# Optimization experiments

Hardware: AMD Instinct MI355X
Metric: run time of the kernel (lower is better)

The kernel has to match this reference:

```python
import jax, jax.numpy as jnp
from jax import lax
import numpy as np

K = 3  # kernel size for both convs


def setup_inputs() -> dict:
    key = jax.random.key(0)
    k1, k2, k3, k4, k5 = jax.random.split(key, 5)
    x = jax.random.normal(k1, (8, 3, 384, 384), dtype=jnp.float32)
    # offset-producing conv: 18 = 2*3*3 offset channels for a 3x3 deform kernel
    w1 = jax.random.normal(k2, (18, 3, K, K), dtype=jnp.float32) * 0.05
    b1 = jax.random.normal(k3, (18,), dtype=jnp.float32) * 0.05
    # deformable conv weight/bias: in=3, out=3, 3x3
    w2 = jax.random.normal(k4, (3, 3, K, K), dtype=jnp.float32) * 0.2
    b2 = jax.random.normal(k5, (3,), dtype=jnp.float32) * 0.05
    return {"x": x, "w1": w1, "b1": b1, "w2": w2, "b2": b2}


def _deform_conv2d(x, offset, w, b):
    # x: [B,C,H,W], offset: [B, 2*K*K, Ho, Wo] (per-tap (dy,dx) interleaved),
    # w: [Co,C,K,K], b: [Co]. stride=1, pad=0, dilation=1, zero-padding bilinear.
    B, C, H, W = x.shape
    KK = K * K
    Ho, Wo = H - (K - 1), W - (K - 1)
    off = offset.reshape(B, KK, 2, Ho, Wo)
    dy, dx = off[:, :, 0], off[:, :, 1]                      # [B,KK,Ho,Wo]

    kh = jnp.repeat(jnp.arange(K, dtype=jnp.float32), K)     # [KK] kernel row
    kw = jnp.tile(jnp.arange(K, dtype=jnp.float32), K)       # [KK] kernel col
    base_y = jnp.arange(Ho, dtype=jnp.float32)[None, :, None] + kh[:, None, None]  # [KK,Ho,1]
    base_x = jnp.arange(Wo, dtype=jnp.float32)[None, None, :] + kw[:, None, None]  # [KK,1,Wo]
    py = base_y[None] + dy                                   # [B,KK,Ho,Wo]
    px = base_x[None] + dx

    y0 = jnp.floor(py)
    x0 = jnp.floor(px)
    wy = py - y0
    wx = px - x0

    x_flat = x.reshape(B, C, H * W)
    N = KK * Ho * Wo

    def gather_corner(yc, xc, wgt):
        valid = (yc >= 0) & (yc <= H - 1) & (xc >= 0) & (xc <= W - 1)
        yi = jnp.clip(yc, 0, H - 1).astype(jnp.int32)
        xi = jnp.clip(xc, 0, W - 1).astype(jnp.int32)
        idx = (yi * W + xi).reshape(B, 1, N)
        g = jnp.take_along_axis(x_flat, idx, axis=2)          # [B,C,N]
        return g * (wgt * valid.astype(x.dtype)).reshape(B, 1, N)

    val = gather_corner(y0, x0, (1 - wy) * (1 - wx))
    val = val + gather_corner(y0, x0 + 1, (1 - wy) * wx)
    val = val + gather_corner(y0 + 1, x0, wy * (1 - wx))
    val = val + gather_corner(y0 + 1, x0 + 1, wy * wx)
    val = val.reshape(B, C, KK, Ho, Wo)

    out = jnp.einsum('bckhw,ock->bohw', val, w.reshape(w.shape[0], C, KK))
    return out + b[None, :, None, None]


def reference(x, w1, b1, w2, b2):
    offset = lax.conv_general_dilated(
        x, w1, window_strides=(1, 1), padding='VALID',
        dimension_numbers=('NCHW', 'OIHW', 'NCHW')) + b1[None, :, None, None]
    return _deform_conv2d(x, offset, w2, b2)
```

## Files before the change

kernel.cpp:

```cpp
#include <hip/hip_runtime.h>


#define BB 8
#define HH 384
#define WW 384
#define HO 382
#define WO 382
#define HW (HH * WW)
#define TW 64
#define TH 4
#define TILES_X 6
#define TILES_Y 96
#define SROWS 11
#define SCOLS 72
#define SSTRIDE 73

typedef float v2f __attribute__((ext_vector_type(2), aligned(4)));
typedef float v4f __attribute__((ext_vector_type(4), aligned(16)));

static __device__ __forceinline__ v2f fma2(v2f a, v2f b, v2f c) {
    return __builtin_elementwise_fma(a, b, c);
}
static __device__ __forceinline__ v4f fma4(v4f a, v4f b, v4f c) {
    return __builtin_elementwise_fma(a, b, c);
}

__global__ __launch_bounds__(256) void deform_tiled(
    const float* __restrict__ x,
    const float* __restrict__ w1,
    const float* __restrict__ b1,
    const float* __restrict__ w2,
    const float* __restrict__ b2,
    float* __restrict__ out)
{
    __shared__ v4f  s_tile[SROWS * SSTRIDE];
    __shared__ float s_w1p[486];
    __shared__ float s_b1[18];
    __shared__ float s_w2p[54];
    __shared__ float s_w2s[27];
    __shared__ float s_b2[3];

    for (int i = threadIdx.x; i < 486; i += 256) {
        const int oc = i / 27, rem = i % 27, c = rem / 9, j = rem % 9;
        const int k = oc >> 1, comp = oc & 1;
        s_w1p[((j * 3 + c) * 9 + k) * 2 + comp] = w1[i];
    }
    if (threadIdx.x < 81) {
        const int i = threadIdx.x;
        const int o = i / 27, c = (i % 27) / 9, k = i % 9;
        if (o < 2) s_w2p[(k * 3 + c) * 2 + o] = w2[i];
        else       s_w2s[k * 3 + c] = w2[i];
    }
    if (threadIdx.x < 18) s_b1[threadIdx.x] = b1[threadIdx.x];
    if (threadIdx.x < 3)  s_b2[threadIdx.x] = b2[threadIdx.x];

    const int b  = blockIdx.x & 7;
    const int t  = blockIdx.x >> 3;
    const int tx = t % TILES_X;
    const int ty = t / TILES_X;
    const int w0 = tx * TW;
    const int r0 = ty * TH;

    const float* xp0 = x + (long)b * 3 * HW;
    const float* xp1 = xp0 + HW;
    const float* xp2 = xp0 + 2 * HW;

    const int gr0 = r0 - 2, gc0 = w0 - 2;
    for (int s = threadIdx.x; s < SROWS * SCOLS; s += 256) {
        const int sr = s / SCOLS, sc = s - sr * SCOLS;
        const int gy = min(max(gr0 + sr, 0), HH - 1);
        const int gx = min(max(gc0 + sc, 0), WW - 1);
        const int base = gy * WW + gx;
        v4f v;
        v.x = xp0[base];
        v.y = xp1[base];
        v.z = xp2[base];
        v.w = 0.f;
        s_tile[sr * SSTRIDE + sc] = v;
    }
    __syncthreads();

    const int wo_in = threadIdx.x & 63;
    const int ho_in = threadIdx.x >> 6;
    const int wo = w0 + wo_in;
    const int ho = r0 + ho_in;
    if (wo >= WO || ho >= HO) return;

    v2f off2[9];
#pragma unroll
    for (int k = 0; k < 9; ++k) {
        v2f v; v.x = s_b1[2 * k]; v.y = s_b1[2 * k + 1];
        off2[k] = v;
    }

    const v2f* w1p = (const v2f*)s_w1p;
#pragma unroll
    for (int j = 0; j < 9; ++j) {
        const int i = j / 3, jj = j % 3;
        const v4f q = s_tile[(ho_in + 2 + i) * SSTRIDE + (wo_in + 2 + jj)];
#pragma unroll
        for (int c = 0; c < 3; ++c) {
            const float xc = (c == 0) ? q.x : (c == 1) ? q.y : q.z;
            v2f xcv; xcv.x = xc; xcv.y = xc;
            const v2f* wrow = w1p + (j * 3 + c) * 9;
#pragma unroll
            for (int k = 0; k < 9; ++k)
                off2[k] = fma2(xcv, wrow[k], off2[k]);
        }
    }

    float acc0 = s_b2[0], acc1 = s_b2[1], acc2 = s_b2[2];
    const v2f* w2p = (const v2f*)s_w2p;

    const bool interior = (gr0 >= 0) & (gc0 >= 0) &
                          (gr0 + SROWS <= HH) & (gc0 + SCOLS <= WW);

    if (interior) {
#pragma unroll 1
        for (int k = 0; k < 9; ++k) {
            const int kh = k / 3, kw = k - kh * 3;
            v2f pos; pos.x = (float)(ho + kh); pos.y = (float)(wo + kw);
            pos += off2[k];
            const v2f fl = __builtin_elementwise_floor(pos);
            const v2f fr = pos - fl;
            const int y0 = (int)fl.x;
            const int x0 = (int)fl.y;

            const int ly0 = y0 - gr0;
            const int lx  = x0 - gc0;
            const bool inTile = ((unsigned)ly0 <= SROWS - 2) &
                                ((unsigned)lx  <= SCOLS - 2);

            float g00 = (1.f - fr.x) * (1.f - fr.y);
            float g01 = (1.f - fr.x) * fr.y;
            float g10 = fr.x * (1.f - fr.y);
            float g11 = fr.x * fr.y;

            const int cy0 = min(max(ly0, 0), SROWS - 2);
            const int cx  = min(max(lx, 0),  SCOLS - 2);
            const v4f* p0 = s_tile + cy0 * SSTRIDE + cx;
            const v4f* p1 = p0 + SSTRIDE;
            v4f q00 = p0[0], q01 = p0[1];
            v4f q10 = p1[0], q11 = p1[1];

            if (!inTile) {
                const int ry0 = min(max(y0, 0), HH - 1);
                const int ry1 = min(max(y0 + 1, 0), HH - 1);
                const int xbs = min(max(x0, 0), WW - 2);
                const bool vy0 = (y0 >= 0) & (y0 <= HH - 1);
                const bool vy1 = (y0 >= -1) & (y0 <= HH - 2);
                const bool vx0 = (x0 >= 0) & (x0 <= WW - 1);
                const bool vx1 = (x0 >= -1) & (x0 <= WW - 2);
                const float wy0m = vy0 ? (1.f - fr.x) : 0.f;
                const float wy1m = vy1 ? fr.x : 0.f;
                const float wx0m = vx0 ? (1.f - fr.y) : 0.f;
                const float wx1m = vx1 ? fr.y : 0.f;
                const bool selA = (x0 >= WW - 1);
                const bool selB = (x0 >= 0);
                const float e0 = (selA ? 0.f : wx0m) + (selB ? 0.f : wx1m);
                const float e1 = (selA ? wx0m : 0.f) + (selB ? wx1m : 0.f);
                g00 = wy0m * e0; g01 = wy0m * e1;
                g10 = wy1m * e0; g11 = wy1m * e1;
                const int o0 = ry0 * WW + xbs;
                const int o1 = ry1 * WW + xbs;
                q00.x = xp0[o0];     q00.y = xp1[o0];     q00.z = xp2[o0];
                q01.x = xp0[o0 + 1]; q01.y = xp1[o0 + 1]; q01.z = xp2[o0 + 1];
                q10.x = xp0[o1];     q10.y = xp1[o1];     q10.z = xp2[o1];
                q11.x = xp0[o1 + 1]; q11.y = xp1[o1 + 1]; q11.z = xp2[o1 + 1];
            }

            v4f gv; gv.x = g00; gv.y = g00; gv.z = g00; gv.w = g00;
            v4f t4 = gv * q00;
            gv.x = g01; gv.y = g01; gv.z = g01; gv.w = g01;
            t4 = fma4(gv, q01, t4);
            gv.x = g10; gv.y = g10; gv.z = g10; gv.w = g10;
            t4 = fma4(gv, q10, t4);
            gv.x = g11; gv.y = g11; gv.z = g11; gv.w = g11;
            t4 = fma4(gv, q11, t4);

            const float v0 = t4.x, v1 = t4.y, v2v = t4.z;

            v2f acc01; acc01.x = acc0; acc01.y = acc1;
            v2f vv;
            vv.x = v0;  vv.y = v0;  acc01 = fma2(vv, w2p[k * 3 + 0], acc01);
            vv.x = v1;  vv.y = v1;  acc01 = fma2(vv, w2p[k * 3 + 1], acc01);
            vv.x = v2v; vv.y = v2v; acc01 = fma2(vv, w2p[k * 3 + 2], acc01);
            acc0 = acc01.x; acc1 = acc01.y;
            acc2 = fmaf(s_w2s[k * 3 + 0], v0, acc2);
            acc2 = fmaf(s_w2s[k * 3 + 1], v1, acc2);
            acc2 = fmaf(s_w2s[k * 3 + 2], v2v, acc2);
        }
    } else {
#pragma unroll 1
        for (int k = 0; k < 9; ++k) {
            const int kh = k / 3, kw = k - kh * 3;
            v2f pos; pos.x = (float)(ho + kh); pos.y = (float)(wo + kw);
            pos += off2[k];
            const v2f fl = __builtin_elementwise_floor(pos);
            const v2f fr = pos - fl;
            const int y0 = (int)fl.x;
            const int x0 = (int)fl.y;

            const int ry0 = min(max(y0, 0), HH - 1);
            const int ry1 = min(max(y0 + 1, 0), HH - 1);
            const int xbs = min(max(x0, 0), WW - 2);

            const bool vy0 = (y0 >= 0) & (y0 <= HH - 1);
            const bool vy1 = (y0 >= -1) & (y0 <= HH - 2);
            const bool vx0 = (x0 >= 0) & (x0 <= WW - 1);
            const bool vx1 = (x0 >= -1) & (x0 <= WW - 2);
            const float wy0m = vy0 ? (1.f - fr.x) : 0.f;
            const float wy1m = vy1 ? fr.x : 0.f;
            const float wx0m = vx0 ? (1.f - fr.y) : 0.f;
            const float wx1m = vx1 ? fr.y : 0.f;

            const bool selA = (x0 >= WW - 1);
            const bool selB = (x0 >= 0);
            const float e0 = (selA ? 0.f : wx0m) + (selB ? 0.f : wx1m);
            const float e1 = (selA ? wx0m : 0.f) + (selB ? wx1m : 0.f);
            const float g00 = wy0m * e0, g01 = wy0m * e1;
            const float g10 = wy1m * e0, g11 = wy1m * e1;

            const int ly0 = ry0 - gr0;
            const int ly1 = ry1 - gr0;
            const int lx  = xbs - gc0;
            const bool inTile = ((unsigned)ly0 <= SROWS - 1) &
                                ((unsigned)ly1 <= SROWS - 1) &
                                ((unsigned)lx  <= SCOLS - 2);

            const int cy0 = min(max(ly0, 0), SROWS - 1);
            const int cy1 = min(max(ly1, 0), SROWS - 1);
            const int cx  = min(max(lx, 0),  SCOLS - 2);
            const v4f* p0 = s_tile + cy0 * SSTRIDE + cx;
            const v4f* p1 = s_tile + cy1 * SSTRIDE + cx;
            v4f q00 = p0[0], q01 = p0[1];
            v4f q10 = p1[0], q11 = p1[1];

            if (!inTile) {
                const int o0 = ry0 * WW + xbs;
                const int o1 = ry1 * WW + xbs;
                q00.x = xp0[o0];     q00.y = xp1[o0];     q00.z = xp2[o0];
                q01.x = xp0[o0 + 1]; q01.y = xp1[o0 + 1]; q01.z = xp2[o0 + 1];
                q10.x = xp0[o1];     q10.y = xp1[o1];     q10.z = xp2[o1];
                q11.x = xp0[o1 + 1]; q11.y = xp1[o1 + 1]; q11.z = xp2[o1 + 1];
            }

            v4f gv; gv.x = g00; gv.y = g00; gv.z = g00; gv.w = g00;
            v4f t4 = gv * q00;
            gv.x = g01; gv.y = g01; gv.z = g01; gv.w = g01;
            t4 = fma4(gv, q01, t4);
            gv.x = g10; gv.y = g10; gv.z = g10; gv.w = g10;
            t4 = fma4(gv, q10, t4);
            gv.x = g11; gv.y = g11; gv.z = g11; gv.w = g11;
            t4 = fma4(gv, q11, t4);

            const float v0 = t4.x, v1 = t4.y, v2v = t4.z;

            v2f acc01; acc01.x = acc0; acc01.y = acc1;
            v2f vv;
            vv.x = v0;  vv.y = v0;  acc01 = fma2(vv, w2p[k * 3 + 0], acc01);
            vv.x = v1;  vv.y = v1;  acc01 = fma2(vv, w2p[k * 3 + 1], acc01);
            vv.x = v2v; vv.y = v2v; acc01 = fma2(vv, w2p[k * 3 + 2], acc01);
            acc0 = acc01.x; acc1 = acc01.y;
            acc2 = fmaf(s_w2s[k * 3 + 0], v0, acc2);
            acc2 = fmaf(s_w2s[k * 3 + 1], v1, acc2);
            acc2 = fmaf(s_w2s[k * 3 + 2], v2v, acc2);
        }
    }

    const long obase = ((long)(b * 3) * HO + ho) * WO + wo;
    __builtin_nontemporal_store(acc0, out + obase);
    __builtin_nontemporal_store(acc1, out + obase + (long)HO * WO);
    __builtin_nontemporal_store(acc2, out + obase + 2L * HO * WO);
}

extern "C" void kernel_launch(void* const* d_in, const int* in_sizes, int n_in,
                              void* d_out, int out_size, void* d_ws, size_t ws_size,
                              hipStream_t stream) {
    const float* x  = (const float*)d_in[0];
    const float* w1 = (const float*)d_in[1];
    const float* b1 = (const float*)d_in[2];
    const float* w2 = (const float*)d_in[3];
    const float* b2 = (const float*)d_in[4];
    float* out = (float*)d_out;

    const int blocks = TILES_X * TILES_Y * BB;
    deform_tiled<<<blocks, 256, 0, stream>>>(x, w1, b1, w2, b2, out);
}
```

Before: 110.8 us.

## Use 32x8 tiles and defer out-of-tile taps to a correction pass

Changes the block tile from 64x4 to 32x8 outputs, which gives a squarer shared-memory halo (15x39) and drops the padded stride. The interior path now fully unrolls the 9-tap loop using only shared-memory samples and records out-of-tile taps in a bitmask. A rare second pass then recomputes those taps from global memory and adds the difference between the correct and the clamped shared-memory value. This removes the divergent branch from the hot loop so the compiler can schedule the taps freely, at the cost of recomputing rare taps and possible LDS bank conflicts now that the stride is 39 instead of 73.

New measurement: 109.6 us, median of 2. About the same (-1.1%).

```diff
diff --git a/kernel.cpp b/kernel.cpp
--- a/kernel.cpp
+++ b/kernel.cpp
@@ -7,13 +7,13 @@
 #define HO 382
 #define WO 382
 #define HW (HH * WW)
-#define TW 64
-#define TH 4
-#define TILES_X 6
-#define TILES_Y 96
-#define SROWS 11
-#define SCOLS 72
-#define SSTRIDE 73
+#define TW 32
+#define TH 8
+#define TILES_X 12
+#define TILES_Y 48
+#define SROWS 15
+#define SCOLS 39
+#define SSTRIDE 39
 
 typedef float v2f __attribute__((ext_vector_type(2), aligned(4)));
 typedef float v4f __attribute__((ext_vector_type(4), aligned(16)));
@@ -80,8 +80,8 @@
     }
     __syncthreads();
 
-    const int wo_in = threadIdx.x & 63;
-    const int ho_in = threadIdx.x >> 6;
+    const int wo_in = threadIdx.x & 31;
+    const int ho_in = threadIdx.x >> 5;
     const int wo = w0 + wo_in;
     const int ho = r0 + ho_in;
     if (wo >= WO || ho >= HO) return;
@@ -116,7 +116,8 @@
                           (gr0 + SROWS <= HH) & (gc0 + SCOLS <= WW);
 
     if (interior) {
-#pragma unroll 1
+        unsigned bad = 0u;
+#pragma unroll
         for (int k = 0; k < 9; ++k) {
             const int kh = k / 3, kw = k - kh * 3;
             v2f pos; pos.x = (float)(ho + kh); pos.y = (float)(wo + kw);
@@ -125,49 +126,23 @@
             const v2f fr = pos - fl;
             const int y0 = (int)fl.x;
             const int x0 = (int)fl.y;
-
             const int ly0 = y0 - gr0;
             const int lx  = x0 - gc0;
-            const bool inTile = ((unsigned)ly0 <= SROWS - 2) &
-                                ((unsigned)lx  <= SCOLS - 2);
-
-            float g00 = (1.f - fr.x) * (1.f - fr.y);
-            float g01 = (1.f - fr.x) * fr.y;
-            float g10 = fr.x * (1.f - fr.y);
-            float g11 = fr.x * fr.y;
+
+            bad |= (((unsigned)ly0 > (unsigned)(SROWS - 2)) |
+                    ((unsigned)lx  > (unsigned)(SCOLS - 2))) ? (1u << k) : 0u;
+
+            const float g00 = (1.f - fr.x) * (1.f - fr.y);
+            const float g01 = (1.f - fr.x) * fr.y;
+            const float g10 = fr.x * (1.f - fr.y);
+            const float g11 = fr.x * fr.y;
 
             const int cy0 = min(max(ly0, 0), SROWS - 2);
             const int cx  = min(max(lx, 0),  SCOLS - 2);
             const v4f* p0 = s_tile + cy0 * SSTRIDE + cx;
             const v4f* p1 = p0 + SSTRIDE;
-            v4f q00 = p0[0], q01 = p0[1];
-            v4f q10 = p1[0], q11 = p1[1];
-
-            if (!inTile) {
-                const int ry0 = min(max(y0, 0), HH - 1);
-                const int ry1 = min(max(y0 + 1, 0), HH - 1);
-                const int xbs = min(max(x0, 0), WW - 2);
-                const bool vy0 = (y0 >= 0) & (y0 <= HH - 1);
-                const bool vy1 = (y0 >= -1) & (y0 <= HH - 2);
-                const bool vx0 = (x0 >= 0) & (x0 <= WW - 1);
-                const bool vx1 = (x0 >= -1) & (x0 <= WW - 2);
-                const float wy0m = vy0 ? (1.f - fr.x) : 0.f;
-                const float wy1m = vy1 ? fr.x : 0.f;
-                const float wx0m = vx0 ? (1.f - fr.y) : 0.f;
-                const float wx1m = vx1 ? fr.y : 0.f;
-                const bool selA = (x0 >= WW - 1);
-                const bool selB = (x0 >= 0);
-                const float e0 = (selA ? 0.f : wx0m) + (selB ? 0.f : wx1m);
-                const float e1 = (selA ? wx0m : 0.f) + (selB ? wx1m : 0.f);
-                g00 = wy0m * e0; g01 = wy0m * e1;
-                g10 = wy1m * e0; g11 = wy1m * e1;
-                const int o0 = ry0 * WW + xbs;
-                const int o1 = ry1 * WW + xbs;
-                q00.x = xp0[o0];     q00.y = xp1[o0];     q00.z = xp2[o0];
-                q01.x = xp0[o0 + 1]; q01.y = xp1[o0 + 1]; q01.z = xp2[o0 + 1];
-                q10.x = xp0[o1];     q10.y = xp1[o1];     q10.z = xp2[o1];
-                q11.x = xp0[o1 + 1]; q11.y = xp1[o1 + 1]; q11.z = xp2[o1 + 1];
-            }
+            const v4f q00 = p0[0], q01 = p0[1];
+            const v4f q10 = p1[0], q11 = p1[1];
 
             v4f gv; gv.x = g00; gv.y = g00; gv.z = g00; gv.w = g00;
             v4f t4 = gv * q00;
@@ -189,6 +164,89 @@
             acc2 = fmaf(s_w2s[k * 3 + 0], v0, acc2);
             acc2 = fmaf(s_w2s[k * 3 + 1], v1, acc2);
             acc2 = fmaf(s_w2s[k * 3 + 2], v2v, acc2);
+        }
+
+        if (bad) {
+#pragma unroll 1
+            for (int k = 0; k < 9; ++k) {
+                if ((bad >> k) & 1u) {
+                    const int kh = k / 3, kw = k - kh * 3;
+                    v2f pos; pos.x = (float)(ho + kh); pos.y = (float)(wo + kw);
+                    pos += off2[k];
+                    const v2f fl = __builtin_elementwise_floor(pos);
+                    const v2f fr = pos - fl;
+                    const int y0 = (int)fl.x;
+                    const int x0 = (int)fl.y;
+
+                    const int ly0 = y0 - gr0;
+                    const int lx  = x0 - gc0;
+                    const float a00 = (1.f - fr.x) * (1.f - fr.y);
+                    const float a01 = (1.f - fr.x) * fr.y;
+                    const float a10 = fr.x * (1.f - fr.y);
+                    const float a11 = fr.x * fr.y;
+                    const int cy0 = min(max(ly0, 0), SROWS - 2);
+                    const int cx  = min(max(lx, 0),  SCOLS - 2);
+                    const v4f* p0 = s_tile + cy0 * SSTRIDE + cx;
+                    const v4f* p1 = p0 + SSTRIDE;
+                    const v4f w00v = p0[0], w01v = p0[1];
+                    const v4f w10v = p1[0], w11v = p1[1];
+                    v4f gv; gv.x = a00; gv.y = a00; gv.z = a00; gv.w = a00;
+                    v4f tw = gv * w00v;
+                    gv.x = a01; gv.y = a01; gv.z = a01; gv.w = a01;
+                    tw = fma4(gv, w01v, tw);
+                    gv.x = a10; gv.y = a10; gv.z = a10; gv.w = a10;
+                    tw = fma4(gv, w10v, tw);
+                    gv.x = a11; gv.y = a11; gv.z = a11; gv.w = a11;
+                    tw = fma4(gv, w11v, tw);
+
+                    const int ry0 = min(max(y0, 0), HH - 1);
+                    const int ry1 = min(max(y0 + 1, 0), HH - 1);
+                    const int xbs = min(max(x0, 0), WW - 2);
+                    const bool vy0 = (y0 >= 0) & (y0 <= HH - 1);
+                    const bool vy1 = (y0 >= -1) & (y0 <= HH - 2);
+                    const bool vx0 = (x0 >= 0) & (x0 <= WW - 1);
+                    const bool vx1 = (x0 >= -1) & (x0 <= WW - 2);
+                    const float wy0m = vy0 ? (1.f - fr.x) : 0.f;
+                    const float wy1m = vy1 ? fr.x : 0.f;
+                    const float wx0m = vx0 ? (1.f - fr.y) : 0.f;
+                    const float wx1m = vx1 ? fr.y : 0.f;
+                    const bool selA = (x0 >= WW - 1);
+                    const bool selB = (x0 >= 0);
+                    const float e0 = (selA ? 0.f : wx0m) + (selB ? 0.f : wx1m);
+                    const float e1 = (selA ? wx0m : 0.f) + (selB ? wx1m : 0.f);
+                    const float g00 = wy0m * e0, g01 = wy0m * e1;
+                    const float g10 = wy1m * e0, g11 = wy1m * e1;
+                    const int o0 = ry0 * WW + xbs;
+                    const int o1 = ry1 * WW + xbs;
+                    v4f q00, q01, q10, q11;
+                    q00.x = xp0[o0];     q00.y = xp1[o0];     q00.z = xp2[o0];     q00.w = 0.f;
+                    q01.x = xp0[o0 + 1]; q01.y = xp1[o0 + 1]; q01.z = xp2[o0 + 1]; q01.w = 0.f;
+                    q10.x = xp0[o1];     q10.y = xp1[o1];     q10.z = xp2[o1];     q10.w = 0.f;
+                    q11.x = xp0[o1 + 1]; q11.y = xp1[o1 + 1]; q11.z = xp2[o1 + 1]; q11.w = 0.f;
+                    gv.x = g00; gv.y = g00; gv.z = g00; gv.w = g00;
+                    v4f tr = gv * q00;
+                    gv.x = g01; gv.y = g01; gv.z = g01; gv.w = g01;
+                    tr = fma4(gv, q01, tr);
+                    gv.x = g10; gv.y = g10; gv.z = g10; gv.w = g10;
+                    tr = fma4(gv, q10, tr);
+                    gv.x = g11; gv.y = g11; gv.z = g11; gv.w = g11;
+                    tr = fma4(gv, q11, tr);
+
+                    const float d0 = tr.x - tw.x;
+                    const float d1 = tr.y - tw.y;
+                    const float d2 = tr.z - tw.z;
+
+                    v2f acc01; acc01.x = acc0; acc01.y = acc1;
+                    v2f vv;
+                    vv.x = d0; vv.y = d0; acc01 = fma2(vv, w2p[k * 3 + 0], acc01);
+                    vv.x = d1; vv.y = d1; acc01 = fma2(vv, w2p[k * 3 + 1], acc01);
+                    vv.x = d2; vv.y = d2; acc01 = fma2(vv, w2p[k * 3 + 2], acc01);
+                    acc0 = acc01.x; acc1 = acc01.y;
+                    acc2 = fmaf(s_w2s[k * 3 + 0], d0, acc2);
+                    acc2 = fmaf(s_w2s[k * 3 + 1], d1, acc2);
+                    acc2 = fmaf(s_w2s[k * 3 + 2], d2, acc2);
+                }
+            }
         }
     } else {
 #pragma unroll 1
```
